# Performance work log

Measured on AMD Instinct MI355X. Metric: run time of the kernel, lower is better.

The kernel has to match this reference:

```python
import jax, jax.numpy as jnp
import numpy as np

N = 1_000_000   # total nodes
H = 128         # hidden_dim
B = 16_384      # num graphs in batch


def setup_inputs() -> dict:
    key = jax.random.key(0)
    k0, k1, k2, k3 = jax.random.split(key, 4)
    x = jax.random.normal(k0, (N, H), dtype=jnp.float32)
    batch_index = jnp.sort(jax.random.randint(k1, (N,), 0, B))
    s = 1.0 / np.sqrt(H)
    W1 = jax.random.normal(k2, (H, H), dtype=jnp.float32) * s
    b1 = jnp.zeros((H,), dtype=jnp.float32)
    W2 = jax.random.normal(k3, (H, 1), dtype=jnp.float32) * s
    b2 = jnp.zeros((1,), dtype=jnp.float32)
    return {"x": x, "W1": W1, "b1": b1, "W2": W2, "b2": b2,
            "batch_index": batch_index, "num_graphs": B}


def reference(x, W1, b1, W2, b2, batch_index, num_graphs):
    # --- global mean pool ---
    seg_sum = jax.ops.segment_sum(x, batch_index, num_segments=num_graphs)
    counts = jax.ops.segment_sum(jnp.ones((x.shape[0],), x.dtype), batch_index,
                                 num_segments=num_graphs)
    mean = seg_sum / jnp.maximum(counts, 1.0)[:, None]          # [B, H]
    # --- global max pool ---
    mx = jax.ops.segment_max(x, batch_index, num_segments=num_graphs)  # [B, H]
    # --- attentional aggregation: gate MLP -> segment softmax -> weighted sum ---
    h = jax.nn.silu(x @ W1 + b1)                                # [N, H]
    gate = (h @ W2 + b2)[:, 0]                                  # [N]
    gmax = jax.ops.segment_max(gate, batch_index, num_segments=num_graphs)
    e = jnp.exp(gate - gmax[batch_index])
    denom = jax.ops.segment_sum(e, batch_index, num_segments=num_graphs)
    att = e / denom[batch_index]                                # [N] per-segment softmax
    attn_out = jax.ops.segment_sum(att[:, None] * x, batch_index,
                                   num_segments=num_graphs)     # [B, H]
    return jnp.concatenate([mean, mx, attn_out], axis=-1)       # [B, 3H]
```

## Files before the change

kernel.cpp:

```cpp
#include <hip/hip_runtime.h>
#include <hip/hip_bf16.h>
#include <math.h>

#define H 128
#define TILE 64
#define XB_STRIDE 136
#define PB_STRIDE 68

typedef __attribute__((ext_vector_type(8))) short bf16x8;
typedef __attribute__((ext_vector_type(4))) float f32x4;

__device__ __forceinline__ short f2bf(float f) {
  union { float f; unsigned u; } v; v.f = f;
  unsigned r = v.u + 0x7fffu + ((v.u >> 16) & 1u);
  return (short)(r >> 16);
}

__global__ void prep_kernel(const float* __restrict__ w1, short* __restrict__ w1t) {
  int i = blockIdx.x * blockDim.x + threadIdx.x;
  if (i >= H * H) return;
  int k = i >> 7, n = i & (H - 1);
  w1t[n * H + k] = f2bf(w1[k * H + n]);
}

__global__ void bounds_kernel(const int* __restrict__ bi, int* __restrict__ seg_start,
                              int N, int B) {
  int n = blockIdx.x * blockDim.x + threadIdx.x;
  if (n >= N) return;
  int cur = bi[n];
  int prev = (n == 0) ? -1 : bi[n - 1];
  for (int g = prev + 1; g <= cur; ++g) seg_start[g] = n;
  if (n == N - 1) {
    for (int g = cur + 1; g <= B; ++g) seg_start[g] = N;
  }
}

__global__ __launch_bounds__(256) void fused_kernel(
    const float* __restrict__ x, const short* __restrict__ w1t,
    const float* __restrict__ b1, const float* __restrict__ w2,
    const float* __restrict__ b2, const int* __restrict__ seg_start,
    float* __restrict__ out)
{
  __shared__ __align__(16) short xb[TILE * XB_STRIDE];
  __shared__ __align__(16) float pbuf[TILE * PB_STRIDE];
  __shared__ float w_lds[TILE];
  __shared__ float bc2[2];

  const int g = blockIdx.x;
  const int s = seg_start[g];
  const int e = seg_start[g + 1];
  const int R = e - s;

  const int tid  = threadIdx.x;
  const int w    = tid >> 6;
  const int lane = tid & 63;
  const int l15  = lane & 15;
  const int q    = lane >> 4;

  const int c4 = (tid & 31) * 4;
  const int rb = tid >> 5;

  float4 sum4 = make_float4(0.f, 0.f, 0.f, 0.f);
  float4 mx4  = make_float4(-INFINITY, -INFINITY, -INFINITY, -INFINITY);
  float4 av4  = make_float4(0.f, 0.f, 0.f, 0.f);
  float m_run = -INFINITY, l_run = 0.f;

  const float b2v  = b2[0];
  const int   c0   = 32 * w + l15, c1 = c0 + 16;
  const float w2c0 = w2[c0], w2c1 = w2[c1];
  const float b1c0 = b1[c0], b1c1 = b1[c1];

  for (int t0 = 0; t0 < R; t0 += TILE) {
    const int Rt    = min(TILE, R - t0);
    const int mtMax = (Rt + 15) >> 4;

#pragma unroll
    for (int i = 0; i < 8; ++i) {
      const int row = rb + 8 * i;
      float4 v = make_float4(0.f, 0.f, 0.f, 0.f);
      if (row < Rt) v = *(const float4*)(x + (size_t)(s + t0 + row) * H + c4);
      short4 sv = make_short4(f2bf(v.x), f2bf(v.y), f2bf(v.z), f2bf(v.w));
      *(short4*)(&xb[row * XB_STRIDE + c4]) = sv;
    }
    __syncthreads();

    f32x4 acc[4][2] = {};
#pragma unroll
    for (int kc = 0; kc < H; kc += 32) {
      bf16x8 a[4], b[2];
#pragma unroll
      for (int mt = 0; mt < 4; ++mt)
        if (mt < mtMax)
          a[mt] = *(const bf16x8*)(&xb[(16 * mt + l15) * XB_STRIDE + kc + 8 * q]);
#pragma unroll
      for (int nt = 0; nt < 2; ++nt) {
        int n = 32 * w + 16 * nt + l15;
        b[nt] = *(const bf16x8*)(w1t + n * H + kc + 8 * q);
      }
#pragma unroll
      for (int mt = 0; mt < 4; ++mt)
        if (mt < mtMax)
#pragma unroll
          for (int nt = 0; nt < 2; ++nt)
            acc[mt][nt] = __builtin_amdgcn_mfma_f32_16x16x32_bf16(a[mt], b[nt], acc[mt][nt], 0, 0, 0);
    }

#pragma unroll
    for (int mt = 0; mt < 4; ++mt) {
      if (mt < mtMax) {
#pragma unroll
        for (int r = 0; r < 4; ++r) {
          float h0 = acc[mt][0][r] + b1c0;
          float h1 = acc[mt][1][r] + b1c1;
          float s0 = h0 / (1.0f + __expf(-h0));
          float s1 = h1 / (1.0f + __expf(-h1));
          pbuf[(16 * mt + 4 * q + r) * PB_STRIDE + 16 * w + l15] = s0 * w2c0 + s1 * w2c1;
        }
      }
    }
    __syncthreads();

    if (tid < 64) {
      const int row = tid;
      float4 t4 = make_float4(0.f, 0.f, 0.f, 0.f);
#pragma unroll
      for (int j = 0; j < 16; ++j) {
        float4 pv = *(const float4*)(&pbuf[row * PB_STRIDE + 4 * j]);
        t4.x += pv.x; t4.y += pv.y; t4.z += pv.z; t4.w += pv.w;
      }
      const float gate = (t4.x + t4.y) + (t4.z + t4.w) + b2v;
      const bool valid = row < Rt;
      float gm = valid ? gate : -INFINITY;
#pragma unroll
      for (int m = 1; m < 64; m <<= 1) gm = fmaxf(gm, __shfl_xor(gm, m));
      const float m_new = fmaxf(m_run, gm);
      const float wv = valid ? __expf(gate - m_new) : 0.f;
      w_lds[row] = wv;
      float tl = wv;
#pragma unroll
      for (int m = 1; m < 64; m <<= 1) tl += __shfl_xor(tl, m);
      if (tid == 0) { bc2[0] = m_new; bc2[1] = tl; }
    }
    __syncthreads();

    const float m_new = bc2[0];
    const float tl    = bc2[1];
    const float corr  = __expf(m_run - m_new);
    m_run = m_new;
    l_run = l_run * corr + tl;
    av4.x *= corr; av4.y *= corr; av4.z *= corr; av4.w *= corr;
#pragma unroll
    for (int i = 0; i < 8; ++i) {
      const int row = rb + 8 * i;
      if (row < Rt) {
        const float4 v = *(const float4*)(x + (size_t)(s + t0 + row) * H + c4);
        const float wv = w_lds[row];
        sum4.x += v.x; sum4.y += v.y; sum4.z += v.z; sum4.w += v.w;
        mx4.x = fmaxf(mx4.x, v.x); mx4.y = fmaxf(mx4.y, v.y);
        mx4.z = fmaxf(mx4.z, v.z); mx4.w = fmaxf(mx4.w, v.w);
        av4.x += wv * v.x; av4.y += wv * v.y;
        av4.z += wv * v.z; av4.w += wv * v.w;
      }
    }
  }

  float* mb = pbuf;
  {
    const int base = rb * 136 + c4;
    *(float4*)(&mb[       base]) = sum4;
    *(float4*)(&mb[1088 + base]) = mx4;
    *(float4*)(&mb[2176 + base]) = av4;
  }
  __syncthreads();
  if (tid < H) {
    const int c = tid;
    float sv = 0.f, mv = -INFINITY, av = 0.f;
#pragma unroll
    for (int r8 = 0; r8 < 8; ++r8) {
      sv += mb[r8 * 136 + c];
      mv  = fmaxf(mv, mb[1088 + r8 * 136 + c]);
      av += mb[2176 + r8 * 136 + c];
    }
    float* og = out + (size_t)g * (3 * H);
    og[c]         = sv / fmaxf((float)R, 1.0f);
    og[H + c]     = mv;
    og[2 * H + c] = (R > 0) ? (av / l_run) : 0.0f;
  }
}

extern "C" void kernel_launch(void* const* d_in, const int* in_sizes, int n_in,
                              void* d_out, int out_size, void* d_ws, size_t ws_size,
                              hipStream_t stream)
{
  const float* x   = (const float*)d_in[0];
  const float* w1  = (const float*)d_in[1];
  const float* b1  = (const float*)d_in[2];
  const float* w2  = (const float*)d_in[3];
  const float* b2  = (const float*)d_in[4];
  const int*  bidx = (const int*)d_in[5];

  const int N  = in_sizes[5];
  const int Bn = out_size / (3 * H);

  char* ws = (char*)d_ws;
  size_t off = 0;
  int* seg_start = (int*)(ws + off);
  off += (size_t)(Bn + 1) * sizeof(int);
  off = (off + 255) & ~(size_t)255;
  short* w1t = (short*)(ws + off);

  prep_kernel<<<(H * H + 255) / 256, 256, 0, stream>>>(w1, w1t);
  bounds_kernel<<<(N + 255) / 256, 256, 0, stream>>>(bidx, seg_start, N, Bn);
  fused_kernel<<<Bn, 256, 0, stream>>>(x, w1t, b1, w2, b2, seg_start, (float*)d_out);
}
```

Baseline: 930.3 us.

## Use 512-thread blocks, shuffle-reduce gate, and fold sum/max into load pass

The block grows to 512 threads (8 waves), with each wave owning 16 output columns of the gate MLP. Partial gate dot-products are reduced with in-wave shuffles instead of a 64-wide LDS buffer. Every wave now runs the per-row softmax redundantly, which removes one block barrier and the LDS broadcast. Sum and max pooling are folded into the first x load, and LDS shrinks so more blocks fit per CU, at the cost of more shuffles and duplicated softmax work.

```diff
diff --git a/kernel.cpp b/kernel.cpp
--- a/kernel.cpp
+++ b/kernel.cpp
@@ -5,7 +5,8 @@
 #define H 128
 #define TILE 64
 #define XB_STRIDE 136
-#define PB_STRIDE 68
+#define WB_STRIDE 9
+#define MB_STRIDE 136
 
 typedef __attribute__((ext_vector_type(8))) short bf16x8;
 typedef __attribute__((ext_vector_type(4))) float f32x4;
@@ -35,21 +36,20 @@
   }
 }
 
-__global__ __launch_bounds__(256) void fused_kernel(
+__global__ __launch_bounds__(512, 7) void fused_kernel(
     const float* __restrict__ x, const short* __restrict__ w1t,
     const float* __restrict__ b1, const float* __restrict__ w2,
     const float* __restrict__ b2, const int* __restrict__ seg_start,
     float* __restrict__ out)
 {
-  __shared__ __align__(16) short xb[TILE * XB_STRIDE];
-  __shared__ __align__(16) float pbuf[TILE * PB_STRIDE];
-  __shared__ float w_lds[TILE];
-  __shared__ float bc2[2];
+  __shared__ __align__(16) char smem[3 * 16 * MB_STRIDE * 4];
+  short* xb   = (short*)smem;
+  float* wbuf = (float*)(smem + TILE * XB_STRIDE * 2);
+  float* mb   = (float*)smem;
 
   const int g = blockIdx.x;
   const int s = seg_start[g];
-  const int e = seg_start[g + 1];
-  const int R = e - s;
+  const int R = seg_start[g + 1] - s;
 
   const int tid  = threadIdx.x;
   const int w    = tid >> 6;
@@ -66,120 +66,112 @@
   float m_run = -INFINITY, l_run = 0.f;
 
   const float b2v  = b2[0];
-  const int   c0   = 32 * w + l15, c1 = c0 + 16;
-  const float w2c0 = w2[c0], w2c1 = w2[c1];
-  const float b1c0 = b1[c0], b1c1 = b1[c1];
+  const int   c0   = 16 * w + l15;
+  const float w2c0 = w2[c0];
+  const float b1c0 = b1[c0];
+
+  const float* xp = x + (size_t)s * H + c4;
 
   for (int t0 = 0; t0 < R; t0 += TILE) {
     const int Rt    = min(TILE, R - t0);
     const int mtMax = (Rt + 15) >> 4;
-
-#pragma unroll
-    for (int i = 0; i < 8; ++i) {
-      const int row = rb + 8 * i;
+    const float* xt = xp + (size_t)t0 * H;
+
+#pragma unroll
+    for (int i = 0; i < 4; ++i) {
+      const int row = rb + 16 * i;
       float4 v = make_float4(0.f, 0.f, 0.f, 0.f);
-      if (row < Rt) v = *(const float4*)(x + (size_t)(s + t0 + row) * H + c4);
-      short4 sv = make_short4(f2bf(v.x), f2bf(v.y), f2bf(v.z), f2bf(v.w));
-      *(short4*)(&xb[row * XB_STRIDE + c4]) = sv;
-    }
-    __syncthreads();
-
-    f32x4 acc[4][2] = {};
-#pragma unroll
-    for (int kc = 0; kc < H; kc += 32) {
-      bf16x8 a[4], b[2];
-#pragma unroll
-      for (int mt = 0; mt < 4; ++mt)
-        if (mt < mtMax)
-          a[mt] = *(const bf16x8*)(&xb[(16 * mt + l15) * XB_STRIDE + kc + 8 * q]);
-#pragma unroll
-      for (int nt = 0; nt < 2; ++nt) {
-        int n = 32 * w + 16 * nt + l15;
-        b[nt] = *(const bf16x8*)(w1t + n * H + kc + 8 * q);
-      }
-#pragma unroll
-      for (int mt = 0; mt < 4; ++mt)
-        if (mt < mtMax)
-#pragma unroll
-          for (int nt = 0; nt < 2; ++nt)
-            acc[mt][nt] = __builtin_amdgcn_mfma_f32_16x16x32_bf16(a[mt], b[nt], acc[mt][nt], 0, 0, 0);
-    }
-
-#pragma unroll
-    for (int mt = 0; mt < 4; ++mt) {
-      if (mt < mtMax) {
-#pragma unroll
-        for (int r = 0; r < 4; ++r) {
-          float h0 = acc[mt][0][r] + b1c0;
-          float h1 = acc[mt][1][r] + b1c1;
-          float s0 = h0 / (1.0f + __expf(-h0));
-          float s1 = h1 / (1.0f + __expf(-h1));
-          pbuf[(16 * mt + 4 * q + r) * PB_STRIDE + 16 * w + l15] = s0 * w2c0 + s1 * w2c1;
-        }
-      }
-    }
-    __syncthreads();
-
-    if (tid < 64) {
-      const int row = tid;
-      float4 t4 = make_float4(0.f, 0.f, 0.f, 0.f);
-#pragma unroll
-      for (int j = 0; j < 16; ++j) {
-        float4 pv = *(const float4*)(&pbuf[row * PB_STRIDE + 4 * j]);
-        t4.x += pv.x; t4.y += pv.y; t4.z += pv.z; t4.w += pv.w;
-      }
-      const float gate = (t4.x + t4.y) + (t4.z + t4.w) + b2v;
-      const bool valid = row < Rt;
-      float gm = valid ? gate : -INFINITY;
-#pragma unroll
-      for (int m = 1; m < 64; m <<= 1) gm = fmaxf(gm, __shfl_xor(gm, m));
-      const float m_new = fmaxf(m_run, gm);
-      const float wv = valid ? __expf(gate - m_new) : 0.f;
-      w_lds[row] = wv;
-      float tl = wv;
-#pragma unroll
-      for (int m = 1; m < 64; m <<= 1) tl += __shfl_xor(tl, m);
-      if (tid == 0) { bc2[0] = m_new; bc2[1] = tl; }
-    }
-    __syncthreads();
-
-    const float m_new = bc2[0];
-    const float tl    = bc2[1];
-    const float corr  = __expf(m_run - m_new);
-    m_run = m_new;
-    l_run = l_run * corr + tl;
-    av4.x *= corr; av4.y *= corr; av4.z *= corr; av4.w *= corr;
-#pragma unroll
-    for (int i = 0; i < 8; ++i) {
-      const int row = rb + 8 * i;
       if (row < Rt) {
-        const float4 v = *(const float4*)(x + (size_t)(s + t0 + row) * H + c4);
-        const float wv = w_lds[row];
+        v = *(const float4*)(xt + (size_t)row * H);
         sum4.x += v.x; sum4.y += v.y; sum4.z += v.z; sum4.w += v.w;
         mx4.x = fmaxf(mx4.x, v.x); mx4.y = fmaxf(mx4.y, v.y);
         mx4.z = fmaxf(mx4.z, v.z); mx4.w = fmaxf(mx4.w, v.w);
-        av4.x += wv * v.x; av4.y += wv * v.y;
-        av4.z += wv * v.z; av4.w += wv * v.w;
-      }
-    }
-  }
-
-  float* mb = pbuf;
+      }
+      short4 sv = make_short4(f2bf(v.x), f2bf(v.y), f2bf(v.z), f2bf(v.w));
+      *(short4*)(&xb[row * XB_STRIDE + c4]) = sv;
+    }
+    __syncthreads();
+
+    f32x4 acc[4] = {};
+#pragma unroll
+    for (int kc = 0; kc < H; kc += 32) {
+      const bf16x8 b = *(const bf16x8*)(w1t + c0 * H + kc + 8 * q);
+#pragma unroll
+      for (int mt = 0; mt < 4; ++mt) {
+        if (mt < mtMax) {
+          const bf16x8 a = *(const bf16x8*)(&xb[(16 * mt + l15) * XB_STRIDE + kc + 8 * q]);
+          acc[mt] = __builtin_amdgcn_mfma_f32_16x16x32_bf16(a, b, acc[mt], 0, 0, 0);
+        }
+      }
+    }
+
+#pragma unroll
+    for (int mt = 0; mt < 4; ++mt) {
+      if (mt < mtMax) {
+#pragma unroll
+        for (int r = 0; r < 4; ++r) {
+          float h0 = acc[mt][r] + b1c0;
+          float s0 = h0 / (1.0f + __expf(-h0));
+          float p  = s0 * w2c0;
+          p += __shfl_xor(p, 1);
+          p += __shfl_xor(p, 2);
+          p += __shfl_xor(p, 4);
+          p += __shfl_xor(p, 8);
+          if (l15 == 0) wbuf[(16 * mt + 4 * q + r) * WB_STRIDE + w] = p;
+        }
+      }
+    }
+    __syncthreads();
+
+    {
+      const int row = lane;
+      float gate = b2v;
+#pragma unroll
+      for (int j = 0; j < 8; ++j) gate += wbuf[row * WB_STRIDE + j];
+      const bool valid = row < Rt;
+      float gm = valid ? gate : -INFINITY;
+#pragma unroll
+      for (int m2 = 1; m2 < 64; m2 <<= 1) gm = fmaxf(gm, __shfl_xor(gm, m2));
+      const float m_new = fmaxf(m_run, gm);
+      const float wv = valid ? __expf(gate - m_new) : 0.f;
+      float tl = wv;
+#pragma unroll
+      for (int m2 = 1; m2 < 64; m2 <<= 1) tl += __shfl_xor(tl, m2);
+      const float corr = __expf(m_run - m_new);
+      m_run = m_new;
+      l_run = l_run * corr + tl;
+      av4.x *= corr; av4.y *= corr; av4.z *= corr; av4.w *= corr;
+
+#pragma unroll
+      for (int i = 0; i < 4; ++i) {
+        const int row2 = rb + 16 * i;
+        const float wvi = __shfl(wv, row2);
+        if (row2 < Rt) {
+          const float4 v = *(const float4*)(xt + (size_t)row2 * H);
+          av4.x += wvi * v.x; av4.y += wvi * v.y;
+          av4.z += wvi * v.z; av4.w += wvi * v.w;
+        }
+      }
+    }
+  }
+
+  __syncthreads();
+
   {
-    const int base = rb * 136 + c4;
+    const int base = rb * MB_STRIDE + c4;
     *(float4*)(&mb[       base]) = sum4;
-    *(float4*)(&mb[1088 + base]) = mx4;
-    *(float4*)(&mb[2176 + base]) = av4;
+    *(float4*)(&mb[2176 + base]) = mx4;
+    *(float4*)(&mb[4352 + base]) = av4;
   }
   __syncthreads();
   if (tid < H) {
     const int c = tid;
     float sv = 0.f, mv = -INFINITY, av = 0.f;
 #pragma unroll
-    for (int r8 = 0; r8 < 8; ++r8) {
-      sv += mb[r8 * 136 + c];
-      mv  = fmaxf(mv, mb[1088 + r8 * 136 + c]);
-      av += mb[2176 + r8 * 136 + c];
+    for (int r16 = 0; r16 < 16; ++r16) {
+      sv += mb[r16 * MB_STRIDE + c];
+      mv  = fmaxf(mv, mb[2176 + r16 * MB_STRIDE + c]);
+      av += mb[4352 + r16 * MB_STRIDE + c];
     }
     float* og = out + (size_t)g * (3 * H);
     og[c]         = sv / fmaxf((float)R, 1.0f);
@@ -211,5 +203,5 @@
 
   prep_kernel<<<(H * H + 255) / 256, 256, 0, stream>>>(w1, w1t);
   bounds_kernel<<<(N + 255) / 256, 256, 0, stream>>>(bidx, seg_start, N, Bn);
-  fused_kernel<<<Bn, 256, 0, stream>>>(x, w1t, b1, w2, b2, seg_start, (float*)d_out);
-}
+  fused_kernel<<<Bn, 512, 0, stream>>>(x, w1t, b1, w2, b2, seg_start, (float*)d_out);
+}
```

Result: slower. 2.001 ms (+115.1%).
